# Kernel optimization log

Hardware: AMD Instinct MI355X
Metric: run time of the kernel (lower is better)

## Reference

```python
import jax, jax.numpy as jnp
import numpy as np

K = 3; PAD = 1; STRIDE = 1; EPS = 1e-5


def setup_inputs() -> dict:
    key = jax.random.key(0)
    k0, k1, k2 = jax.random.split(key, 3)
    B, C, H, W, O = 4, 256, 64, 64, 256
    x = jax.random.normal(k0, (B, C, H, W), jnp.float32)
    # offset conv: small random weights so offsets are nontrivial but bounded
    w_off = jax.random.normal(k1, (2 * K * K, C, K, K), jnp.float32) * 0.01
    b_off = jnp.zeros((2 * K * K,), jnp.float32)
    # kaiming normal, mode=fan_out: std = sqrt(2 / (O*K*K))
    w_def = jax.random.normal(k2, (O, C, K, K), jnp.float32) * np.float32(np.sqrt(2.0 / (O * K * K)))
    gamma = jnp.ones((O,), jnp.float32)
    beta = jnp.zeros((O,), jnp.float32)
    return {"x": x, "w_off": w_off, "b_off": b_off, "w_def": w_def, "gamma": gamma, "beta": beta}


def _bilinear_gather(x, py, px):
    """x: [B,C,H,W]; py,px: [B,K2,Ho,Wo] float sample coords.
    Returns [B,K2,Ho,Wo,C] with zero padding outside (per-corner masking,
    matching torchvision deform_conv2d)."""
    B, C, H, W = x.shape
    y0f = jnp.floor(py); x0f = jnp.floor(px)
    wy1 = py - y0f; wy0 = 1.0 - wy1
    wx1 = px - x0f; wx0 = 1.0 - wx1
    bidx = jnp.arange(B)[:, None, None, None]

    def corner(yf, xf, wgt):
        valid = (yf >= 0) & (yf <= H - 1) & (xf >= 0) & (xf <= W - 1)
        yc = jnp.clip(yf.astype(jnp.int32), 0, H - 1)
        xc = jnp.clip(xf.astype(jnp.int32), 0, W - 1)
        v = x[bidx, :, yc, xc]  # [B,K2,Ho,Wo,C] (advanced idx moves C last)
        return v * (wgt * valid)[..., None]

    return (corner(y0f, x0f, wy0 * wx0) + corner(y0f, x0f + 1.0, wy0 * wx1)
            + corner(y0f + 1.0, x0f, wy1 * wx0) + corner(y0f + 1.0, x0f + 1.0, wy1 * wx1))


def _forward(x, w_off, b_off, w_def, gamma, beta):
    B, C, H, W = x.shape
    O = w_def.shape[0]
    K2 = K * K
    # 1) offset-predicting conv
    off = jax.lax.conv_general_dilated(x, w_off, (STRIDE, STRIDE), ((PAD, PAD), (PAD, PAD)))
    off = off + b_off[None, :, None, None]
    Ho, Wo = off.shape[2], off.shape[3]
    off = off.reshape(B, K2, 2, Ho, Wo)  # pairs (dy, dx) per kernel tap
    # 2) deformable sampling locations
    ky, kx = jnp.meshgrid(jnp.arange(K, dtype=jnp.float32), jnp.arange(K, dtype=jnp.float32), indexing='ij')
    base_y = (jnp.arange(Ho, dtype=jnp.float32) * STRIDE - PAD)
    base_x = (jnp.arange(Wo, dtype=jnp.float32) * STRIDE - PAD)
    py = off[:, :, 0] + ky.reshape(K2)[None, :, None, None] + base_y[None, None, :, None]
    px = off[:, :, 1] + kx.reshape(K2)[None, :, None, None] + base_x[None, None, None, :]
    vals = _bilinear_gather(x, py, px)  # [B,K2,Ho,Wo,C]
    # 3) deform conv GEMM (bias=False)
    out = jnp.einsum('bkhwc,ock->bohw', vals, w_def.reshape(O, C, K2))
    # 4) BatchNorm (training mode: batch stats) + ReLU
    mean = out.mean(axis=(0, 2, 3))
    var = out.var(axis=(0, 2, 3))
    out = (out - mean[None, :, None, None]) * (gamma * jax.lax.rsqrt(var + EPS))[None, :, None, None]
    out = out + beta[None, :, None, None]
    return jax.nn.relu(out)


def reference(x, w_off, b_off, w_def, gamma, beta):
    return _forward(x, w_off, b_off, w_def, gamma, beta)
```

## Files before the change

kernel.cpp:

```cpp
#include <hip/hip_runtime.h>
#include <hip/hip_bf16.h>

typedef unsigned int  uint;
typedef unsigned short ushort;
typedef short bf16x8 __attribute__((ext_vector_type(8)));
typedef float f32x4  __attribute__((ext_vector_type(4)));

#define HW   4096
#define KD   2304

__device__ __forceinline__ void load_lds16(const void* g, void* l) {
    __builtin_amdgcn_global_load_lds((const __attribute__((address_space(1))) void*)g,
                                     (__attribute__((address_space(3))) void*)l, 16, 0, 0);
}
__device__ __forceinline__ float blo(uint u) { return __uint_as_float(u << 16); }
__device__ __forceinline__ float bhi(uint u) { return __uint_as_float(u & 0xffff0000u); }
__device__ __forceinline__ uint pack2(float e, float o) {
    __hip_bfloat16 he = __float2bfloat16(e), ho = __float2bfloat16(o);
    return (uint)(*(ushort*)&he) | ((uint)(*(ushort*)&ho) << 16);
}

__global__ void prep_x2t(const float* __restrict__ x, uint* __restrict__ x2t) {
    __shared__ uint tl[32][65];
    int bidx = blockIdx.x;
    int ab  = bidx & 63;
    int cpb = (bidx >> 6) & 3;
    int b   = bidx >> 8;
    int t = threadIdx.x;
#pragma unroll
    for (int i = 0; i < 8; ++i) {
        int idx = i * 256 + t;
        int cp = idx >> 6, a = idx & 63;
        const float* p = x + ((size_t)(b * 256 + (cpb * 32 + cp) * 2)) * HW + ab * 64 + a;
        tl[cp][a] = pack2(p[0], p[HW]);
    }
    __syncthreads();
#pragma unroll
    for (int i = 0; i < 8; ++i) {
        int idx = i * 256 + t;
        int a = idx >> 5, cp = idx & 31;
        x2t[((size_t)b * 4096 + ab * 64 + a) * 128 + cpb * 32 + cp] = tl[cp][a];
    }
}

__global__ void prep_bt(const float* __restrict__ w_def, ushort* __restrict__ bt) {
    int idx = blockIdx.x * 256 + threadIdx.x;
    int c   = idx & 255;
    int tap = (idx >> 8) % 9;
    int o   = idx / KD;
    __hip_bfloat16 h = __float2bfloat16(w_def[(o * 256 + c) * 9 + tap]);
    bt[idx] = *(ushort*)&h;
}

__global__ void prep_bt0(const float* __restrict__ w_off, ushort* __restrict__ bt0) {
    int idx = blockIdx.x * 256 + threadIdx.x;
    int c   = idx & 255;
    int tap = (idx >> 8) % 9;
    int j   = idx / KD;
    float v = (j < 18) ? w_off[(j * 256 + c) * 9 + tap] : 0.f;
    __hip_bfloat16 h = __float2bfloat16(v);
    bt0[idx] = *(ushort*)&h;
}

__global__ __launch_bounds__(512) void gemm_off(const uint* __restrict__ x2t,
                                                const ushort* __restrict__ bt0,
                                                const float* __restrict__ b_off,
                                                float* __restrict__ off) {
    int id = blockIdx.x;
    int xcd = id & 7;
    int b = xcd >> 1, h = (xcd & 1) * 32 + (id >> 3);
    int t = threadIdx.x, wv = t >> 6, lane = t & 63;
    int mrow = lane & 15, quad = lane >> 4;
    int mq = wv & 3, nn = wv >> 2;

    __shared__ uint   lX[3 * 64 * 32];
    __shared__ ushort lB[32 * 576];

    f32x4 acc = {0.f, 0.f, 0.f, 0.f};

    for (int cb = 0; cb < 4; ++cb) {
#pragma unroll
        for (int s = 0; s < 3; ++s) {
            int q   = s * 8 + wv;
            int dy  = q >> 3;
            int y   = h + dy - 1;
            int sub = q & 7;
            int wl  = sub * 8 + (lane >> 3);
            int cps = ((lane & 7) ^ ((lane >> 3) & 7)) * 4;
            if ((unsigned)y < 64u) {
                const uint* src = x2t + ((size_t)(b * 4096 + y * 64 + wl)) * 128 + cb * 32 + cps;
                load_lds16(src, &lX[q * 256]);
            } else {
                uint4 z = {0u, 0u, 0u, 0u};
                *(uint4*)&lX[q * 256 + lane * 4] = z;
            }
        }
#pragma unroll
        for (int s = 0; s < 5; ++s) {
            int q = s * 8 + wv;
            if (q < 36) {
                int e = q * 512 + lane * 8;
                int o  = e / 576;
                int r  = e - o * 576;
                int chp = r >> 3;
                int ch  = chp ^ (o & 7);
                int tap = ch >> 3, k8 = ch & 7;
                const ushort* src = bt0 + (size_t)o * KD + tap * 256 + cb * 64 + k8 * 8;
                load_lds16(src, &lB[q * 512]);
            }
        }
        __syncthreads();

#pragma unroll
        for (int tap = 0; tap < 9; ++tap) {
            int dy = tap / 3, dx = tap % 3;
            int xx = mq * 16 + mrow + dx - 1;
            bool vx = (unsigned)xx < 64u;
            int xc = min(max(xx, 0), 63);
#pragma unroll
            for (int kb = 0; kb < 2; ++kb) {
                int cp0 = kb * 16 + quad * 4;
                uint4 ad = {0u, 0u, 0u, 0u};
                if (vx) ad = *(const uint4*)&lX[dy * 2048 + xc * 32 + (cp0 ^ ((xc & 7) * 4))];
                bf16x8 af = *(bf16x8*)&ad;
                int o = nn * 16 + mrow;
                int chs = (tap * 8 + (((kb * 4 + quad)) ^ (o & 7)));
                bf16x8 bfr = *(const bf16x8*)&lB[o * 576 + chs * 8];
                acc = __builtin_amdgcn_mfma_f32_16x16x32_bf16(af, bfr, acc, 0, 0, 0);
            }
        }
        __syncthreads();
    }
    {
        int o = nn * 16 + mrow;
        float bias = (o < 18) ? b_off[o] : 0.f;
        f32x4 v = acc;
        v.x += bias; v.y += bias; v.z += bias; v.w += bias;
        int wpos = mq * 16 + quad * 4;
        *(f32x4*)(off + ((size_t)(b * 32 + o)) * HW + h * 64 + wpos) = v;
    }
}

__global__ __attribute__((amdgpu_waves_per_eu(4, 4))) __launch_bounds__(1024)
void fused_main(const uint* __restrict__ x2t,
                const ushort* __restrict__ bt,
                const float* __restrict__ off,
                float* __restrict__ out,
                float* __restrict__ stats) {
    int id = blockIdx.x;
    int xcd = id & 7;
    int b = xcd >> 1, h = (xcd & 1) * 32 + (id >> 3);
    int t = threadIdx.x;
    int wv = t >> 6, lane = t & 63;
    int mrow = lane & 15, quad = lane >> 4;
    bool producer = (wv < 8);
    int ppos = (wv << 3) + (lane >> 3);
    int pc8  = lane & 7;
    int wvc  = wv - 8;

    __shared__ int    sAc[4][9][64];
    __shared__ float  sWc[4][9][64];
    __shared__ ushort lA[2][64 * 64];

    for (int i = t; i < 576; i += 1024) {
        int tap = i >> 6, ww = i & 63;
        int hw = h * 64 + ww;
        float oy = off[((size_t)(b * 32 + 2 * tap)) * HW + hw];
        float ox = off[((size_t)(b * 32 + 2 * tap + 1)) * HW + hw];
        float py = oy + (float)(tap / 3 + h - 1);
        float px = ox + (float)(tap % 3 + ww - 1);
        float y0f = floorf(py), x0f = floorf(px);
        float wy1 = py - y0f, wx1 = px - x0f;
        float wy0 = 1.f - wy1, wx0 = 1.f - wx1;
        bool vy0 = (y0f >= 0.f) && (y0f <= 63.f);
        bool vy1 = (y0f >= -1.f) && (y0f <= 62.f);
        bool vx0 = (x0f >= 0.f) && (x0f <= 63.f);
        bool vx1 = (x0f >= -1.f) && (x0f <= 62.f);
        int iy0 = min(max((int)y0f, 0), 63),  iy1 = min(max((int)y0f + 1, 0), 63);
        int ix0 = min(max((int)x0f, 0), 63),  ix1 = min(max((int)x0f + 1, 0), 63);
        sAc[0][tap][ww] = iy0 * 64 + ix0;
        sAc[1][tap][ww] = iy0 * 64 + ix1;
        sAc[2][tap][ww] = iy1 * 64 + ix0;
        sAc[3][tap][ww] = iy1 * 64 + ix1;
        sWc[0][tap][ww] = wy0 * wx0 * (float)(vy0 && vx0);
        sWc[1][tap][ww] = wy0 * wx1 * (float)(vy0 && vx1);
        sWc[2][tap][ww] = wy1 * wx0 * (float)(vy1 && vx0);
        sWc[3][tap][ww] = wy1 * wx1 * (float)(vy1 && vx1);
    }
    __syncthreads();

    f32x4 acc[4][2];
#pragma unroll
    for (int m = 0; m < 4; ++m)
#pragma unroll
        for (int n = 0; n < 2; ++n) acc[m][n] = {0.f, 0.f, 0.f, 0.f};

    const uint* xb = x2t + (size_t)b * 4096 * 128;

    auto issue_gathers = [&](int sl, uint4 (&g)[4]) {
        int tap = sl >> 2, cb = sl & 3;
        const uint* xp = xb + cb * 32 + pc8 * 4;
        g[0] = *(const uint4*)(xp + (size_t)sAc[0][tap][ppos] * 128);
        g[1] = *(const uint4*)(xp + (size_t)sAc[1][tap][ppos] * 128);
        g[2] = *(const uint4*)(xp + (size_t)sAc[2][tap][ppos] * 128);
        g[3] = *(const uint4*)(xp + (size_t)sAc[3][tap][ppos] * 128);
    };
    auto finish = [&](int sl, ushort* lAb, const uint4 (&g)[4]) {
        int tap = sl >> 2;
        float f0 = sWc[0][tap][ppos], f1 = sWc[1][tap][ppos];
        float f2 = sWc[2][tap][ppos], f3 = sWc[3][tap][ppos];
        const uint* c0 = (const uint*)&g[0];
        const uint* c1 = (const uint*)&g[1];
        const uint* c2 = (const uint*)&g[2];
        const uint* c3 = (const uint*)&g[3];
        uint r[4];
#pragma unroll
        for (int j = 0; j < 4; ++j) {
            float ev = f0 * blo(c0[j]) + f1 * blo(c1[j]) + f2 * blo(c2[j]) + f3 * blo(c3[j]);
            float ov = f0 * bhi(c0[j]) + f1 * bhi(c1[j]) + f2 * bhi(c2[j]) + f3 * bhi(c3[j]);
            r[j] = pack2(ev, ov);
        }
        uint4 gg = {r[0], r[1], r[2], r[3]};
        *(uint4*)&lAb[ppos * 64 + ((pc8 ^ (ppos & 7)) * 8)] = gg;
    };
    auto loadB = [&](int sl, bf16x8 (&br)[4]) {
        int tap = sl >> 2, cb = sl & 3;
        const ushort* base = bt + tap * 256 + cb * 64 + quad * 8;
#pragma unroll
        for (int kb = 0; kb < 2; ++kb)
#pragma unroll
            for (int n = 0; n < 2; ++n) {
                int r = wvc * 32 + n * 16 + mrow;
                br[kb * 2 + n] = *(const bf16x8*)(base + (size_t)r * KD + kb * 32);
            }
    };
    auto mfma_pass = [&](int bi, const bf16x8 (&br)[4]) {
#pragma unroll
        for (int kb = 0; kb < 2; ++kb) {
            bf16x8 af[4];
#pragma unroll
            for (int m = 0; m < 4; ++m) {
                int r = m * 16 + mrow;
                af[m] = *(const bf16x8*)&lA[bi][r * 64 + (((kb * 4 + quad) ^ (r & 7)) * 8)];
            }
#pragma unroll
            for (int n = 0; n < 2; ++n)
#pragma unroll
                for (int m = 0; m < 4; ++m)
                    acc[m][n] = __builtin_amdgcn_mfma_f32_16x16x32_bf16(af[m], br[kb * 2 + n], acc[m][n], 0, 0, 0);
        }
    };

    uint4 gA[4];
    bf16x8 brA[4], brB[4];
    if (producer) {
        issue_gathers(0, gA);
        finish(0, lA[0], gA);
        asm volatile("s_waitcnt lgkmcnt(0)" ::: "memory");
    } else {
        loadB(0, brA);
        loadB(1, brB);
    }
    __builtin_amdgcn_s_barrier();
    __builtin_amdgcn_sched_barrier(0);

    for (int s = 0; s < 36; s += 2) {
        if (producer) {
            issue_gathers(s + 1, gA);
            finish(s + 1, lA[1], gA);
            asm volatile("s_waitcnt lgkmcnt(0)" ::: "memory");
        } else {
            __builtin_amdgcn_s_setprio(1);
            mfma_pass(0, brA);
            __builtin_amdgcn_s_setprio(0);
            if (s + 2 < 36) loadB(s + 2, brA);
        }
        __builtin_amdgcn_s_barrier();
        __builtin_amdgcn_sched_barrier(0);
        if (producer) {
            if (s + 2 < 36) {
                issue_gathers(s + 2, gA);
                finish(s + 2, lA[0], gA);
                asm volatile("s_waitcnt lgkmcnt(0)" ::: "memory");
            }
        } else {
            __builtin_amdgcn_s_setprio(1);
            mfma_pass(1, brB);
            __builtin_amdgcn_s_setprio(0);
            if (s + 3 < 36) loadB(s + 3, brB);
        }
        __builtin_amdgcn_s_barrier();
        __builtin_amdgcn_sched_barrier(0);
    }

    if (!producer) {
#pragma unroll
        for (int n = 0; n < 2; ++n) {
            int o = wvc * 32 + n * 16 + mrow;
            float ss = 0.f, qq = 0.f;
#pragma unroll
            for (int m = 0; m < 4; ++m) {
                int pos = m * 16 + quad * 4;
                f32x4 v = acc[m][n];
                *(f32x4*)(out + ((size_t)(b * 256 + o)) * HW + h * 64 + pos) = v;
                ss += v.x + v.y + v.z + v.w;
                qq += v.x * v.x + v.y * v.y + v.z * v.z + v.w * v.w;
            }
            ss += __shfl_xor(ss, 16); ss += __shfl_xor(ss, 32);
            qq += __shfl_xor(qq, 16); qq += __shfl_xor(qq, 32);
            if (quad == 0) {
                atomicAdd(&stats[o], ss);
                atomicAdd(&stats[512 + o], qq);
            }
        }
    }
}

__global__ void bn_finalize(const float* __restrict__ stats,
                            const float* __restrict__ gamma,
                            float* __restrict__ ms) {
    int o = threadIdx.x;
    float S = stats[o], S2 = stats[512 + o];
    float m  = S / 16384.f;
    float var = S2 / 16384.f - m * m;
    ms[o]       = m;
    ms[256 + o] = gamma[o] * rsqrtf(var + 1e-5f);
}

__global__ void bn_apply(float* __restrict__ out,
                         const float* __restrict__ ms,
                         const float* __restrict__ beta) {
    int idx4 = blockIdx.x * 256 + threadIdx.x;
    int o = (idx4 >> 10) & 255;
    float4 v = ((const float4*)out)[idx4];
    float mu = ms[o], sc = ms[256 + o], be = beta[o];
    v.x = fmaxf((v.x - mu) * sc + be, 0.f);
    v.y = fmaxf((v.y - mu) * sc + be, 0.f);
    v.z = fmaxf((v.z - mu) * sc + be, 0.f);
    v.w = fmaxf((v.w - mu) * sc + be, 0.f);
    ((float4*)out)[idx4] = v;
}

extern "C" void kernel_launch(void* const* d_in, const int* in_sizes, int n_in,
                              void* d_out, int out_size, void* d_ws, size_t ws_size,
                              hipStream_t stream) {
    const float* x     = (const float*)d_in[0];
    const float* w_off = (const float*)d_in[1];
    const float* b_off = (const float*)d_in[2];
    const float* w_def = (const float*)d_in[3];
    const float* gamma = (const float*)d_in[4];
    const float* beta  = (const float*)d_in[5];
    float* out = (float*)d_out;

    char* ws = (char*)d_ws;
    uint*   x2t   = (uint*)ws;
    ushort* bt    = (ushort*)(ws + 8388608);
    ushort* bt0   = (ushort*)(ws + 9568256);
    float*  off   = (float*)(ws + 9715712);
    float*  stats = (float*)(ws + 11812864);
    float*  ms    = (float*)(ws + 11816960);

    hipMemsetAsync(stats, 0, 4096, stream);
    prep_x2t<<<1024, 256, 0, stream>>>(x, x2t);
    prep_bt <<<2304, 256, 0, stream>>>(w_def, bt);
    prep_bt0<<<288,  256, 0, stream>>>(w_off, bt0);
    gemm_off<<<256, 512, 0, stream>>>(x2t, bt0, b_off, off);
    fused_main<<<256, 1024, 0, stream>>>(x2t, bt, off, out, stats);
    bn_finalize<<<1, 256, 0, stream>>>(stats, gamma, ms);
    bn_apply<<<4096, 256, 0, stream>>>(out, ms, beta);
}
```

Baseline: 155.8 us.

## Prefetch gather corners into LDS one stage ahead via direct global-to-LDS loads

Producer waves now issue the four bilinear corner gathers for the next slice directly into a double-buffered LDS staging area with global_load_lds, rather than into registers. Combining is done on the slice loaded earlier, so global gather latency overlaps one full pipeline stage. The cost is an extra 64 KB of LDS, which may reduce occupancy, plus vmcnt bookkeeping that must be right for correctness.

After: 154.9 us. Within noise of the previous version (-0.6%).

```diff
diff --git a/kernel.cpp b/kernel.cpp
--- a/kernel.cpp
+++ b/kernel.cpp
@@ -161,6 +161,7 @@
     __shared__ int    sAc[4][9][64];
     __shared__ float  sWc[4][9][64];
     __shared__ ushort lA[2][64 * 64];
+    __shared__ uint4  cS[2][4][512];
 
     for (int i = t; i < 576; i += 1024) {
         int tap = i >> 6, ww = i & 63;
@@ -197,22 +198,27 @@
 
     const uint* xb = x2t + (size_t)b * 4096 * 128;
 
-    auto issue_gathers = [&](int sl, uint4 (&g)[4]) {
-        int tap = sl >> 2, cb = sl & 3;
+    auto issue_gathers = [&](int sl) {
+        int par = sl & 1, tap = sl >> 2, cb = sl & 3;
         const uint* xp = xb + cb * 32 + pc8 * 4;
-        g[0] = *(const uint4*)(xp + (size_t)sAc[0][tap][ppos] * 128);
-        g[1] = *(const uint4*)(xp + (size_t)sAc[1][tap][ppos] * 128);
-        g[2] = *(const uint4*)(xp + (size_t)sAc[2][tap][ppos] * 128);
-        g[3] = *(const uint4*)(xp + (size_t)sAc[3][tap][ppos] * 128);
+#pragma unroll
+        for (int c = 0; c < 4; ++c) {
+            const uint* src = xp + (size_t)sAc[c][tap][ppos] * 128;
+            load_lds16(src, &cS[par][c][wv * 64]);
+        }
     };
-    auto finish = [&](int sl, ushort* lAb, const uint4 (&g)[4]) {
-        int tap = sl >> 2;
+    auto finish = [&](int sl, ushort* lAb) {
+        int par = sl & 1, tap = sl >> 2;
         float f0 = sWc[0][tap][ppos], f1 = sWc[1][tap][ppos];
         float f2 = sWc[2][tap][ppos], f3 = sWc[3][tap][ppos];
-        const uint* c0 = (const uint*)&g[0];
-        const uint* c1 = (const uint*)&g[1];
-        const uint* c2 = (const uint*)&g[2];
-        const uint* c3 = (const uint*)&g[3];
+        uint4 v0 = cS[par][0][wv * 64 + lane];
+        uint4 v1 = cS[par][1][wv * 64 + lane];
+        uint4 v2 = cS[par][2][wv * 64 + lane];
+        uint4 v3 = cS[par][3][wv * 64 + lane];
+        const uint* c0 = (const uint*)&v0;
+        const uint* c1 = (const uint*)&v1;
+        const uint* c2 = (const uint*)&v2;
+        const uint* c3 = (const uint*)&v3;
         uint r[4];
 #pragma unroll
         for (int j = 0; j < 4; ++j) {
@@ -251,11 +257,13 @@
         }
     };
 
-    uint4 gA[4];
     bf16x8 brA[4], brB[4];
     if (producer) {
-        issue_gathers(0, gA);
-        finish(0, lA[0], gA);
+        issue_gathers(0);
+        issue_gathers(1);
+        asm volatile("s_waitcnt vmcnt(4)" ::: "memory");
+        __builtin_amdgcn_sched_barrier(0);
+        finish(0, lA[0]);
         asm volatile("s_waitcnt lgkmcnt(0)" ::: "memory");
     } else {
         loadB(0, brA);
@@ -266,8 +274,14 @@
 
     for (int s = 0; s < 36; s += 2) {
         if (producer) {
-            issue_gathers(s + 1, gA);
-            finish(s + 1, lA[1], gA);
+            if (s + 2 < 36) {
+                issue_gathers(s + 2);
+                asm volatile("s_waitcnt vmcnt(4)" ::: "memory");
+            } else {
+                asm volatile("s_waitcnt vmcnt(0)" ::: "memory");
+            }
+            __builtin_amdgcn_sched_barrier(0);
+            finish(s + 1, lA[1]);
             asm volatile("s_waitcnt lgkmcnt(0)" ::: "memory");
         } else {
             __builtin_amdgcn_s_setprio(1);
@@ -278,9 +292,15 @@
         __builtin_amdgcn_s_barrier();
         __builtin_amdgcn_sched_barrier(0);
         if (producer) {
+            if (s + 3 < 36) issue_gathers(s + 3);
             if (s + 2 < 36) {
-                issue_gathers(s + 2, gA);
-                finish(s + 2, lA[0], gA);
+                if (s + 3 < 36) {
+                    asm volatile("s_waitcnt vmcnt(4)" ::: "memory");
+                } else {
+                    asm volatile("s_waitcnt vmcnt(0)" ::: "memory");
+                }
+                __builtin_amdgcn_sched_barrier(0);
+                finish(s + 2, lA[0]);
                 asm volatile("s_waitcnt lgkmcnt(0)" ::: "memory");
             }
         } else {
```

## Fuse prep kernels and BN finalize, deepen gather/MFMA pipeline to four buffers

Applied to the files above, without the earlier changes.

Merges the three prep kernels and the stats memset into one launch, and folds BN finalize into bn_apply so each block computes its own channel scale. In the main fused kernel, the A tile buffer grows from two to four stages, so producers gather two k-steps ahead while consumers run two MFMA passes per barrier. The aim is to halve the barriers per iteration and cut launch overhead, at the cost of doubled LDS for A, which could lower occupancy, and some redundant per-block BN arithmetic.

Result: faster. 148.6 us (-4.6%).

```diff
diff --git a/kernel.cpp b/kernel.cpp
--- a/kernel.cpp
+++ b/kernel.cpp
@@ -20,46 +20,53 @@
     return (uint)(*(ushort*)&he) | ((uint)(*(ushort*)&ho) << 16);
 }
 
-__global__ void prep_x2t(const float* __restrict__ x, uint* __restrict__ x2t) {
+__global__ __launch_bounds__(256) void prep_all(const float* __restrict__ x,
+                                                const float* __restrict__ w_def,
+                                                const float* __restrict__ w_off,
+                                                uint* __restrict__ x2t,
+                                                ushort* __restrict__ bt,
+                                                ushort* __restrict__ bt0,
+                                                float* __restrict__ stats) {
     __shared__ uint tl[32][65];
-    int bidx = blockIdx.x;
-    int ab  = bidx & 63;
-    int cpb = (bidx >> 6) & 3;
-    int b   = bidx >> 8;
+    int bid = blockIdx.x;
     int t = threadIdx.x;
-#pragma unroll
-    for (int i = 0; i < 8; ++i) {
-        int idx = i * 256 + t;
-        int cp = idx >> 6, a = idx & 63;
-        const float* p = x + ((size_t)(b * 256 + (cpb * 32 + cp) * 2)) * HW + ab * 64 + a;
-        tl[cp][a] = pack2(p[0], p[HW]);
-    }
-    __syncthreads();
-#pragma unroll
-    for (int i = 0; i < 8; ++i) {
-        int idx = i * 256 + t;
-        int a = idx >> 5, cp = idx & 31;
-        x2t[((size_t)b * 4096 + ab * 64 + a) * 128 + cpb * 32 + cp] = tl[cp][a];
-    }
-}
-
-__global__ void prep_bt(const float* __restrict__ w_def, ushort* __restrict__ bt) {
-    int idx = blockIdx.x * 256 + threadIdx.x;
-    int c   = idx & 255;
-    int tap = (idx >> 8) % 9;
-    int o   = idx / KD;
-    __hip_bfloat16 h = __float2bfloat16(w_def[(o * 256 + c) * 9 + tap]);
-    bt[idx] = *(ushort*)&h;
-}
-
-__global__ void prep_bt0(const float* __restrict__ w_off, ushort* __restrict__ bt0) {
-    int idx = blockIdx.x * 256 + threadIdx.x;
-    int c   = idx & 255;
-    int tap = (idx >> 8) % 9;
-    int j   = idx / KD;
-    float v = (j < 18) ? w_off[(j * 256 + c) * 9 + tap] : 0.f;
-    __hip_bfloat16 h = __float2bfloat16(v);
-    bt0[idx] = *(ushort*)&h;
+    if (bid < 1024) {
+        int ab  = bid & 63;
+        int cpb = (bid >> 6) & 3;
+        int b   = bid >> 8;
+#pragma unroll
+        for (int i = 0; i < 8; ++i) {
+            int idx = i * 256 + t;
+            int cp = idx >> 6, a = idx & 63;
+            const float* p = x + ((size_t)(b * 256 + (cpb * 32 + cp) * 2)) * HW + ab * 64 + a;
+            tl[cp][a] = pack2(p[0], p[HW]);
+        }
+        __syncthreads();
+#pragma unroll
+        for (int i = 0; i < 8; ++i) {
+            int idx = i * 256 + t;
+            int a = idx >> 5, cp = idx & 31;
+            x2t[((size_t)b * 4096 + ab * 64 + a) * 128 + cpb * 32 + cp] = tl[cp][a];
+        }
+    } else if (bid < 3328) {
+        int idx = (bid - 1024) * 256 + t;
+        int c   = idx & 255;
+        int tap = (idx >> 8) % 9;
+        int o   = idx / KD;
+        __hip_bfloat16 h = __float2bfloat16(w_def[(o * 256 + c) * 9 + tap]);
+        bt[idx] = *(ushort*)&h;
+    } else if (bid < 3616) {
+        int idx = (bid - 3328) * 256 + t;
+        int c   = idx & 255;
+        int tap = (idx >> 8) % 9;
+        int j   = idx / KD;
+        float v = (j < 18) ? w_off[(j * 256 + c) * 9 + tap] : 0.f;
+        __hip_bfloat16 h = __float2bfloat16(v);
+        bt0[idx] = *(ushort*)&h;
+    } else {
+        float4 z = {0.f, 0.f, 0.f, 0.f};
+        ((float4*)stats)[t] = z;
+    }
 }
 
 __global__ __launch_bounds__(512) void gemm_off(const uint* __restrict__ x2t,
@@ -160,7 +167,7 @@
 
     __shared__ int    sAc[4][9][64];
     __shared__ float  sWc[4][9][64];
-    __shared__ ushort lA[2][64 * 64];
+    __shared__ ushort lA[4][64 * 64];
 
     for (int i = t; i < 576; i += 1024) {
         int tap = i >> 6, ww = i & 63;
@@ -256,6 +263,8 @@
     if (producer) {
         issue_gathers(0, gA);
         finish(0, lA[0], gA);
+        issue_gathers(1, gA);
+        finish(1, lA[1], gA);
         asm volatile("s_waitcnt lgkmcnt(0)" ::: "memory");
     } else {
         loadB(0, brA);
@@ -266,27 +275,19 @@
 
     for (int s = 0; s < 36; s += 2) {
         if (producer) {
-            issue_gathers(s + 1, gA);
-            finish(s + 1, lA[1], gA);
-            asm volatile("s_waitcnt lgkmcnt(0)" ::: "memory");
+            if (s + 2 < 36) {
+                issue_gathers(s + 2, gA);
+                finish(s + 2, lA[(s + 2) & 3], gA);
+                issue_gathers(s + 3, gA);
+                finish(s + 3, lA[(s + 3) & 3], gA);
+                asm volatile("s_waitcnt lgkmcnt(0)" ::: "memory");
+            }
         } else {
             __builtin_amdgcn_s_setprio(1);
-            mfma_pass(0, brA);
+            mfma_pass(s & 3, brA);
+            mfma_pass((s + 1) & 3, brB);
             __builtin_amdgcn_s_setprio(0);
             if (s + 2 < 36) loadB(s + 2, brA);
-        }
-        __builtin_amdgcn_s_barrier();
-        __builtin_amdgcn_sched_barrier(0);
-        if (producer) {
-            if (s + 2 < 36) {
-                issue_gathers(s + 2, gA);
-                finish(s + 2, lA[0], gA);
-                asm volatile("s_waitcnt lgkmcnt(0)" ::: "memory");
-            }
-        } else {
-            __builtin_amdgcn_s_setprio(1);
-            mfma_pass(1, brB);
-            __builtin_amdgcn_s_setprio(0);
             if (s + 3 < 36) loadB(s + 3, brB);
         }
         __builtin_amdgcn_s_barrier();
@@ -316,24 +317,19 @@
     }
 }
 
-__global__ void bn_finalize(const float* __restrict__ stats,
-                            const float* __restrict__ gamma,
-                            float* __restrict__ ms) {
-    int o = threadIdx.x;
+__global__ __launch_bounds__(256) void bn_apply(float* __restrict__ out,
+                                                const float* __restrict__ stats,
+                                                const float* __restrict__ gamma,
+                                                const float* __restrict__ beta) {
+    int bid = blockIdx.x;
+    int o = (bid >> 2) & 255;
     float S = stats[o], S2 = stats[512 + o];
-    float m  = S / 16384.f;
-    float var = S2 / 16384.f - m * m;
-    ms[o]       = m;
-    ms[256 + o] = gamma[o] * rsqrtf(var + 1e-5f);
-}
-
-__global__ void bn_apply(float* __restrict__ out,
-                         const float* __restrict__ ms,
-                         const float* __restrict__ beta) {
-    int idx4 = blockIdx.x * 256 + threadIdx.x;
-    int o = (idx4 >> 10) & 255;
+    float mu  = S * (1.f / 16384.f);
+    float var = S2 * (1.f / 16384.f) - mu * mu;
+    float sc  = gamma[o] * rsqrtf(var + 1e-5f);
+    float be  = beta[o];
+    int idx4 = bid * 256 + threadIdx.x;
     float4 v = ((const float4*)out)[idx4];
-    float mu = ms[o], sc = ms[256 + o], be = beta[o];
     v.x = fmaxf((v.x - mu) * sc + be, 0.f);
     v.y = fmaxf((v.y - mu) * sc + be, 0.f);
     v.z = fmaxf((v.z - mu) * sc + be, 0.f);
@@ -358,14 +354,9 @@
     ushort* bt0   = (ushort*)(ws + 9568256);
     float*  off   = (float*)(ws + 9715712);
     float*  stats = (float*)(ws + 11812864);
-    float*  ms    = (float*)(ws + 11816960);
-
-    hipMemsetAsync(stats, 0, 4096, stream);
-    prep_x2t<<<1024, 256, 0, stream>>>(x, x2t);
-    prep_bt <<<2304, 256, 0, stream>>>(w_def, bt);
-    prep_bt0<<<288,  256, 0, stream>>>(w_off, bt0);
-    gemm_off<<<256, 512, 0, stream>>>(x2t, bt0, b_off, off);
+
+    prep_all  <<<3617, 256, 0, stream>>>(x, w_def, w_off, x2t, bt, bt0, stats);
+    gemm_off  <<<256, 512, 0, stream>>>(x2t, bt0, b_off, off);
     fused_main<<<256, 1024, 0, stream>>>(x2t, bt, off, out, stats);
-    bn_finalize<<<1, 256, 0, stream>>>(stats, gamma, ms);
-    bn_apply<<<4096, 256, 0, stream>>>(out, ms, beta);
-}
+    bn_apply  <<<4096, 256, 0, stream>>>(out, stats, gamma, beta);
+}
```
